# Kernel tuning notes

Measured on AMD Instinct MI355X. Metric: run time of the kernel, lower is better.

Reference implementation:

```python
import jax, jax.numpy as jnp
import numpy as np

D_MODEL = 1024
N_HEADS = 16
WINDOW = 64
GLOBAL_RATIO = 0.1
HEAD_DIM = D_MODEL // N_HEADS
NEG_INF = -1e9  # matches torch float32 branch of _get_neg_inf
B, L = 1, 2048


def setup_inputs() -> dict:
    key = jax.random.key(0)
    ks = jax.random.split(key, 6)
    x = jax.random.normal(ks[0], (B, L, D_MODEL), jnp.float32)
    s = 1.0 / np.sqrt(D_MODEL)  # nn.Linear default init bound

    def lin(k):
        k1, k2 = jax.random.split(k)
        W = jax.random.uniform(k1, (D_MODEL, D_MODEL), jnp.float32, -s, s)
        b = jax.random.uniform(k2, (D_MODEL,), jnp.float32, -s, s)
        return W, b

    Wq, bq = lin(ks[1])
    Wk, bk = lin(ks[2])
    Wv, bv = lin(ks[3])
    Wo, bo = lin(ks[4])
    n_global = max(1, int(L * GLOBAL_RATIO))  # 204
    global_indices = jnp.sort(jax.random.randint(ks[5], (n_global,), 0, L))
    return dict(x=x, Wq=Wq, bq=bq, Wk=Wk, bk=bk, Wv=Wv, bv=bv, Wo=Wo, bo=bo,
                global_indices=global_indices)


def reference(x, Wq, bq, Wk, bk, Wv, bv, Wo, bo, global_indices):
    Bb, Ll, Dm = x.shape
    H, Dh = N_HEADS, HEAD_DIM
    scale = 1.0 / jnp.sqrt(jnp.float32(Dh))
    # projections (torch Linear: y = x @ W.T + b)
    Q = (x @ Wq.T + bq).reshape(Bb, Ll, H, Dh)
    K = (x @ Wk.T + bk).reshape(Bb, Ll, H, Dh)
    V = (x @ Wv.T + bv).reshape(Bb, Ll, H, Dh)

    # --- local sliding-window attention (vectorized version of the per-i loop) ---
    half = WINDOW // 2
    W = WINDOW + 1  # positions i-half .. i+half inclusive
    pos = jnp.arange(Ll)[:, None] + jnp.arange(-half, half + 1)[None, :]  # [L,W]
    valid = (pos >= 0) & (pos < Ll)          # edge truncation == masking to -inf
    posc = jnp.clip(pos, 0, Ll - 1)
    Kw = K[:, posc]                           # [B,L,W,H,Dh]
    Vw = V[:, posc]
    s_loc = jnp.einsum('blhd,blwhd->bhlw', Q, Kw) * scale
    s_loc = jnp.where(valid[None, None], s_loc, NEG_INF)
    a_loc = jax.nn.softmax(s_loc, axis=-1)
    local = jnp.einsum('bhlw,blwhd->blhd', a_loc, Vw)

    # --- global random-token attention ---
    Kg = K[:, global_indices]                 # [B,G,H,Dh]
    Vg = V[:, global_indices]
    s_g = jnp.einsum('blhd,bghd->bhlg', Q, Kg) * scale
    a_g = jax.nn.softmax(s_g, axis=-1)
    glob = jnp.einsum('bhlg,bghd->blhd', a_g, Vg)

    out = 0.7 * local + 0.3 * glob
    return out.reshape(Bb, Ll, Dm) @ Wo.T + bo
```

## Files before the change

kernel.cpp:

```cpp
#include <hip/hip_runtime.h>
#include <hip/hip_bf16.h>
#include <stdint.h>

#define L_SEQ 2048
#define D_MODEL 1024
#define NH 16
#define DH 64
#define NEG_INF -1e9f

typedef short bf16x4 __attribute__((ext_vector_type(4)));
typedef short bf16x8 __attribute__((ext_vector_type(8)));
typedef float f32x4 __attribute__((ext_vector_type(4)));
typedef unsigned short ushort_t;
typedef const __attribute__((address_space(1))) void* gas_t;
typedef __attribute__((address_space(3))) void* las_t;

#define MFMA16(a, b, c) __builtin_amdgcn_mfma_f32_16x16x32_bf16((a), (b), (c), 0, 0, 0)

__device__ __forceinline__ ushort_t f2b(float f) {
  union { float f; unsigned u; } v; v.f = f;
  unsigned r = v.u + 0x7fffu + ((v.u >> 16) & 1u);
  return (ushort_t)(r >> 16);
}
__device__ __forceinline__ float b2f(ushort_t u) {
  union { unsigned u; float f; } v; v.u = ((unsigned)u) << 16; return v.f;
}

__global__ __launch_bounds__(256) void cvt_kernel(
    const float* __restrict__ x, const float* __restrict__ wq,
    const float* __restrict__ wk, const float* __restrict__ wv,
    const float* __restrict__ wo, ushort_t* __restrict__ out) {
  long e = ((long)blockIdx.x * 256 + threadIdx.x) * 4;
  const float* src; long off;
  if (e < 2097152L)      { src = x;  off = e; }
  else if (e < 3145728L) { src = wq; off = e - 2097152L; }
  else if (e < 4194304L) { src = wk; off = e - 3145728L; }
  else if (e < 5242880L) { src = wv; off = e - 4194304L; }
  else                   { src = wo; off = e - 5242880L; }
  float4 v = *(const float4*)(src + off);
  ushort4 o;
  o.x = f2b(v.x); o.y = f2b(v.y); o.z = f2b(v.z); o.w = f2b(v.w);
  *(ushort4*)(out + e) = o;
}

__global__ __launch_bounds__(512, 4) void gemm_qkv(
    const ushort_t* __restrict__ A, const ushort_t* __restrict__ Wbase,
    const float* __restrict__ b0, const float* __restrict__ b1,
    const float* __restrict__ b2, ushort_t* __restrict__ outbase) {
  const int z = blockIdx.z;
  const ushort_t* W = Wbase + (long)z * (D_MODEL * D_MODEL);
  const float* bias = (z == 0) ? b0 : ((z == 1) ? b1 : b2);
  const float scale = (z == 0) ? 0.125f : 1.0f;

  __shared__ ushort_t As[4 * 128 * 32];
  __shared__ ushort_t Bs[4 * 128 * 32];
  const int tid = threadIdx.x;
  const int lane = tid & 63;
  const int wid = tid >> 6;
  const int wm = wid >> 2, wn = wid & 3;
  const int m0 = blockIdx.x * 128, n0 = blockIdx.y * 128;
  const int K = D_MODEL;
  const int l15 = lane & 15;
  const int lgc = lane >> 4;
  const int xs = (l15 >> 1) & 3;

  const int soff = tid * 16;
  const int srow = soff >> 6;
  const int schunk = (soff >> 4) & 3;
  const int swzcol = ((schunk ^ ((srow >> 1) & 3)) << 3);

  const ushort_t* Aptr = A + (long)(m0 + srow) * K + swzcol;
  const ushort_t* Wptr = W + (long)(n0 + srow) * K + swzcol;

  auto stage = [&](int buf, int step) {
    __builtin_amdgcn_global_load_lds(
        (gas_t)(const void*)(Aptr + step * 32),
        (las_t)(void*)((char*)As + buf * 8192 + soff), 16, 0, 0);
    __builtin_amdgcn_global_load_lds(
        (gas_t)(const void*)(Wptr + step * 32),
        (las_t)(void*)((char*)Bs + buf * 8192 + soff), 16, 0, 0);
  };

  f32x4 acc[4][2] = {};

  auto compute = [&](int buf) {
    const ushort_t* Ab = As + buf * (128 * 32);
    const ushort_t* Bb = Bs + buf * (128 * 32);
    bf16x8 af[4], bf[2];
#pragma unroll
    for (int t = 0; t < 4; ++t)
      af[t] = *(const bf16x8*)(Ab + (wm * 64 + t * 16 + l15) * 32 +
                               ((lgc ^ xs) << 3));
#pragma unroll
    for (int t = 0; t < 2; ++t)
      bf[t] = *(const bf16x8*)(Bb + (wn * 32 + t * 16 + l15) * 32 +
                               ((lgc ^ xs) << 3));
#pragma unroll
    for (int mt = 0; mt < 4; ++mt)
#pragma unroll
      for (int nt = 0; nt < 2; ++nt)
        acc[mt][nt] = MFMA16(af[mt], bf[nt], acc[mt][nt]);
  };

  const int NSTEP = K / 32;
  stage(0, 0);
  stage(1, 1);
  for (int s = 0; s < NSTEP - 2; ++s) {
    stage((s + 2) & 3, s + 2);
    asm volatile("s_waitcnt vmcnt(4)" ::: "memory");
    __builtin_amdgcn_s_barrier();
    __builtin_amdgcn_sched_barrier(0);
    compute(s & 3);
  }
  asm volatile("s_waitcnt vmcnt(2)" ::: "memory");
  __builtin_amdgcn_s_barrier();
  __builtin_amdgcn_sched_barrier(0);
  compute((NSTEP - 2) & 3);
  asm volatile("s_waitcnt vmcnt(0)" ::: "memory");
  __builtin_amdgcn_s_barrier();
  __builtin_amdgcn_sched_barrier(0);
  compute((NSTEP - 1) & 3);

  const int lg4 = (lane >> 4) * 4;
  ushort_t* o = outbase + (long)z * ((long)NH * L_SEQ * DH);
#pragma unroll
  for (int mt = 0; mt < 4; ++mt)
#pragma unroll
    for (int nt = 0; nt < 2; ++nt)
#pragma unroll
      for (int r = 0; r < 4; ++r) {
        int row = m0 + wm * 64 + mt * 16 + lg4 + r;
        int col = n0 + wn * 32 + nt * 16 + l15;
        float v = (acc[mt][nt][r] + bias[col]) * scale;
        o[((long)(col >> 6) * L_SEQ + row) * DH + (col & 63)] = f2b(v);
      }
}

__global__ __launch_bounds__(256, 3) void gemm_out(
    const ushort_t* __restrict__ A, const ushort_t* __restrict__ W,
    const float* __restrict__ bias, float* __restrict__ o) {
  __shared__ ushort_t As[4 * 128 * 32];
  __shared__ ushort_t Bs[4 * 64 * 32];
  const int tid = threadIdx.x;
  const int lane = tid & 63;
  const int wid = tid >> 6;
  const int wm = wid >> 1, wn = wid & 1;
  const int m0 = blockIdx.x * 128, n0 = blockIdx.y * 64;
  const int K = D_MODEL;
  const int l15 = lane & 15;
  const int lgc = lane >> 4;
  const int xs = (l15 >> 1) & 3;

  const int soff = tid * 16;
  const int srow = soff >> 6;
  const int schunk = (soff >> 4) & 3;
  const int swzcol = ((schunk ^ ((srow >> 1) & 3)) << 3);

  const ushort_t* Aptr0 = A + (long)(m0 + srow) * K + swzcol;
  const ushort_t* Aptr1 = A + (long)(m0 + 64 + srow) * K + swzcol;
  const ushort_t* Wptr  = W + (long)(n0 + srow) * K + swzcol;

  auto stage = [&](int buf, int step) {
    __builtin_amdgcn_global_load_lds(
        (gas_t)(const void*)(Aptr0 + step * 32),
        (las_t)(void*)((char*)As + buf * 8192 + soff), 16, 0, 0);
    __builtin_amdgcn_global_load_lds(
        (gas_t)(const void*)(Aptr1 + step * 32),
        (las_t)(void*)((char*)As + buf * 8192 + 4096 + soff), 16, 0, 0);
    __builtin_amdgcn_global_load_lds(
        (gas_t)(const void*)(Wptr + step * 32),
        (las_t)(void*)((char*)Bs + buf * 4096 + soff), 16, 0, 0);
  };

  f32x4 acc[4][2] = {};

  auto compute = [&](int buf) {
    const ushort_t* Ab = As + buf * (128 * 32);
    const ushort_t* Bb = Bs + buf * (64 * 32);
    bf16x8 af[4], bf[2];
#pragma unroll
    for (int t = 0; t < 4; ++t)
      af[t] = *(const bf16x8*)(Ab + (wm * 64 + t * 16 + l15) * 32 +
                               ((lgc ^ xs) << 3));
#pragma unroll
    for (int t = 0; t < 2; ++t)
      bf[t] = *(const bf16x8*)(Bb + (wn * 32 + t * 16 + l15) * 32 +
                               ((lgc ^ xs) << 3));
#pragma unroll
    for (int mt = 0; mt < 4; ++mt)
#pragma unroll
      for (int nt = 0; nt < 2; ++nt)
        acc[mt][nt] = MFMA16(af[mt], bf[nt], acc[mt][nt]);
  };

  const int NSTEP = K / 32;
  stage(0, 0);
  stage(1, 1);
  for (int s = 0; s < NSTEP - 2; ++s) {
    stage((s + 2) & 3, s + 2);
    asm volatile("s_waitcnt vmcnt(6)" ::: "memory");
    __builtin_amdgcn_s_barrier();
    __builtin_amdgcn_sched_barrier(0);
    compute(s & 3);
  }
  asm volatile("s_waitcnt vmcnt(3)" ::: "memory");
  __builtin_amdgcn_s_barrier();
  __builtin_amdgcn_sched_barrier(0);
  compute((NSTEP - 2) & 3);
  asm volatile("s_waitcnt vmcnt(0)" ::: "memory");
  __builtin_amdgcn_s_barrier();
  __builtin_amdgcn_sched_barrier(0);
  compute((NSTEP - 1) & 3);

  const int lg4 = (lane >> 4) * 4;
#pragma unroll
  for (int mt = 0; mt < 4; ++mt)
#pragma unroll
    for (int nt = 0; nt < 2; ++nt)
#pragma unroll
      for (int r = 0; r < 4; ++r) {
        int row = m0 + wm * 64 + mt * 16 + lg4 + r;
        int col = n0 + wn * 32 + nt * 16 + l15;
        o[(long)row * D_MODEL + col] = acc[mt][nt][r] + bias[col];
      }
}

__global__ __launch_bounds__(256) void attn_local(
    const ushort_t* __restrict__ QKV, ushort_t* __restrict__ attnL) {
  __shared__ ushort_t kb[128 * 72];
  __shared__ ushort_t vt[64 * 132];

  const int tid = threadIdx.x;
  const int lane = tid & 63;
  const int w = tid >> 6;
  const int h = blockIdx.y;
  const int q0 = blockIdx.x * 64;

  const long hoff = (long)h * L_SEQ * DH;
  const ushort_t* Qh = QKV + hoff;
  const ushort_t* Kh = QKV + (long)NH * L_SEQ * DH + hoff;
  const ushort_t* Vh = QKV + 2L * NH * L_SEQ * DH + hoff;

  const int rr = tid >> 3;
  const int c8 = (tid & 7) * 8;
  const int l15 = lane & 15, lg = lane >> 4;
  const int ql = q0 + w * 16 + l15;

  int4 vst[4];
#pragma unroll
  for (int it = 0; it < 4; ++it) {
    int r = rr + it * 32;
    int sr = q0 - 32 + r;
    sr = sr < 0 ? 0 : (sr > L_SEQ - 1 ? L_SEQ - 1 : sr);
    vst[it] = *(const int4*)(Vh + (long)sr * DH + c8);
  }
  bf16x8 qf0 = *(const bf16x8*)(Qh + (long)ql * DH + lg * 8);
  bf16x8 qf1 = *(const bf16x8*)(Qh + (long)ql * DH + 32 + lg * 8);

#pragma unroll
  for (int it = 0; it < 4; ++it) {
    int r = rr + it * 32;
    int sr = q0 - 32 + r;
    sr = sr < 0 ? 0 : (sr > L_SEQ - 1 ? L_SEQ - 1 : sr);
    int4 v = *(const int4*)(Kh + (long)sr * DH + c8);
    *(int4*)(kb + r * 72 + c8) = v;
  }
  __syncthreads();

  f32x4 sl[5];
#pragma unroll
  for (int kt = 0; kt < 5; ++kt) {
    f32x4 c = {};
    const ushort_t* kr = kb + (w * 16 + kt * 16 + l15) * 72;
    bf16x8 k0 = *(const bf16x8*)(kr + lg * 8);
    bf16x8 k1 = *(const bf16x8*)(kr + 32 + lg * 8);
    c = MFMA16(k0, qf0, c);
    c = MFMA16(k1, qf1, c);
    sl[kt] = c;
  }

  float mx = NEG_INF;
#pragma unroll
  for (int kt = 0; kt < 5; ++kt)
#pragma unroll
    for (int r4 = 0; r4 < 4; ++r4) {
      int key = q0 - 32 + w * 16 + kt * 16 + lg * 4 + r4;
      int d = key - ql;
      bool valid = (key >= 0) && (key < L_SEQ) && (d <= 32) && (d >= -32);
      float v = valid ? sl[kt][r4] : NEG_INF;
      sl[kt][r4] = v;
      mx = fmaxf(mx, v);
    }
  mx = fmaxf(mx, __shfl_xor(mx, 16, 64));
  mx = fmaxf(mx, __shfl_xor(mx, 32, 64));
  float den = 0.f;
#pragma unroll
  for (int kt = 0; kt < 5; ++kt)
#pragma unroll
    for (int r4 = 0; r4 < 4; ++r4) {
      float e = __expf(sl[kt][r4] - mx);
      sl[kt][r4] = e;
      den += e;
    }
  den += __shfl_xor(den, 16, 64);
  den += __shfl_xor(den, 32, 64);
  const float psl = 0.7f / den;

  bf16x8 pl[3];
#pragma unroll
  for (int s = 0; s < 2; ++s)
#pragma unroll
    for (int j = 0; j < 4; ++j) {
      pl[s][j]     = (short)f2b(sl[2 * s][j] * psl);
      pl[s][j + 4] = (short)f2b(sl[2 * s + 1][j] * psl);
    }
#pragma unroll
  for (int j = 0; j < 4; ++j) {
    pl[2][j]     = (short)f2b(sl[4][j] * psl);
    pl[2][j + 4] = 0;
  }

#pragma unroll
  for (int it = 0; it < 4; ++it) {
    int r = rr + it * 32;
    ushort_t tmp[8]; *(int4*)tmp = vst[it];
#pragma unroll
    for (int j = 0; j < 8; ++j) vt[(c8 + j) * 132 + r] = tmp[j];
  }
  __syncthreads();

#pragma unroll
  for (int dt = 0; dt < 4; ++dt) {
    f32x4 c = {};
    const ushort_t* vrow = vt + (dt * 16 + l15) * 132 + w * 16 + lg * 4;
#pragma unroll
    for (int s = 0; s < 3; ++s) {
      bf16x4 lo = *(const bf16x4*)(vrow + s * 32);
      bf16x4 hi = *(const bf16x4*)(vrow + s * 32 + (s < 2 ? 16 : 0));
      bf16x8 vf = __builtin_shufflevector(lo, hi, 0, 1, 2, 3, 4, 5, 6, 7);
      c = MFMA16(pl[s], vf, c);
    }
#pragma unroll
    for (int r4 = 0; r4 < 4; ++r4) {
      int row = q0 + w * 16 + lg * 4 + r4;
      attnL[(long)row * D_MODEL + h * DH + dt * 16 + l15] = f2b(c[r4]);
    }
  }
}

#define VTW 228
__global__ __launch_bounds__(512) void attn_glob(
    const ushort_t* __restrict__ QKV, const int* __restrict__ gidx, int NG,
    const ushort_t* __restrict__ attnL, ushort_t* __restrict__ attn_out) {
  __shared__ ushort_t kg[208 * 72];
  __shared__ ushort_t vtg[64 * VTW];

  const int tid = threadIdx.x;
  const int lane = tid & 63;
  const int w = tid >> 6;
  const int h = blockIdx.y;
  const int q0 = blockIdx.x * 128;

  const long hoff = (long)h * L_SEQ * DH;
  const ushort_t* Qh = QKV + hoff;
  const ushort_t* Kh = QKV + (long)NH * L_SEQ * DH + hoff;
  const ushort_t* Vh = QKV + 2L * NH * L_SEQ * DH + hoff;

  const int l15 = lane & 15, lg = lane >> 4;
  const int ql = q0 + w * 16 + l15;

  int4 vst[4];
#pragma unroll
  for (int it = 0; it < 4; ++it) {
    int c = tid + it * 512;
    int cl = c < 1664 ? c : 1663;
    int r = cl >> 3, cc = (cl & 7) * 8;
    int idx = r < NG ? r : NG - 1;
    vst[it] = *(const int4*)(Vh + (long)gidx[idx] * DH + cc);
  }
  bf16x8 qf0 = *(const bf16x8*)(Qh + (long)ql * DH + lg * 8);
  bf16x8 qf1 = *(const bf16x8*)(Qh + (long)ql * DH + 32 + lg * 8);
  ushort_t aL[4][4];
#pragma unroll
  for (int dt = 0; dt < 4; ++dt)
#pragma unroll
    for (int r4 = 0; r4 < 4; ++r4) {
      int row = q0 + w * 16 + lg * 4 + r4;
      aL[dt][r4] = attnL[(long)row * D_MODEL + h * DH + dt * 16 + l15];
    }

#pragma unroll
  for (int it = 0; it < 4; ++it) {
    int c = tid + it * 512;
    if (c < 1664) {
      int r = c >> 3, cc = (c & 7) * 8;
      int idx = r < NG ? r : NG - 1;
      int4 v = *(const int4*)(Kh + (long)gidx[idx] * DH + cc);
      *(int4*)(kg + r * 72 + cc) = v;
    }
  }
  __syncthreads();

  f32x4 sg[13];
#pragma unroll
  for (int kt = 0; kt < 13; ++kt) {
    f32x4 c = {};
    bf16x8 k0 = *(const bf16x8*)(kg + (kt * 16 + l15) * 72 + lg * 8);
    bf16x8 k1 = *(const bf16x8*)(kg + (kt * 16 + l15) * 72 + 32 + lg * 8);
    c = MFMA16(k0, qf0, c);
    c = MFMA16(k1, qf1, c);
    sg[kt] = c;
  }

  float mg = NEG_INF;
#pragma unroll
  for (int t = 0; t < 13; ++t)
#pragma unroll
    for (int r4 = 0; r4 < 4; ++r4) {
      int i = t * 16 + lg * 4 + r4;
      float v = (i < NG) ? sg[t][r4] : NEG_INF;
      sg[t][r4] = v;
      mg = fmaxf(mg, v);
    }
  mg = fmaxf(mg, __shfl_xor(mg, 16, 64));
  mg = fmaxf(mg, __shfl_xor(mg, 32, 64));
  float deng = 0.f;
#pragma unroll
  for (int t = 0; t < 13; ++t)
#pragma unroll
    for (int r4 = 0; r4 < 4; ++r4) {
      float e = __expf(sg[t][r4] - mg);
      sg[t][r4] = e;
      deng += e;
    }
  deng += __shfl_xor(deng, 16, 64);
  deng += __shfl_xor(deng, 32, 64);
  const float psg = 0.3f / deng;

  bf16x8 pg[7];
#pragma unroll
  for (int s = 0; s < 6; ++s)
#pragma unroll
    for (int j = 0; j < 4; ++j) {
      pg[s][j]     = (short)f2b(sg[2 * s][j] * psg);
      pg[s][j + 4] = (short)f2b(sg[2 * s + 1][j] * psg);
    }
#pragma unroll
  for (int j = 0; j < 4; ++j) {
    pg[6][j]     = (short)f2b(sg[12][j] * psg);
    pg[6][j + 4] = 0;
  }

#pragma unroll
  for (int it = 0; it < 4; ++it) {
    int c = tid + it * 512;
    if (c < 1664) {
      int r = c >> 3, cc = (c & 7) * 8;
      ushort_t tmp[8]; *(int4*)tmp = vst[it];
#pragma unroll
      for (int j = 0; j < 8; ++j) vtg[(cc + j) * VTW + r] = tmp[j];
    }
  }
  for (int i = tid; i < 64 * 20; i += 512)
    vtg[(i / 20) * VTW + 208 + (i % 20)] = 0;
  __syncthreads();

#pragma unroll
  for (int dt = 0; dt < 4; ++dt) {
    f32x4 c = {};
    const ushort_t* vrow = vtg + (dt * 16 + l15) * VTW + lg * 4;
#pragma unroll
    for (int s = 0; s < 7; ++s) {
      bf16x4 lo = *(const bf16x4*)(vrow + s * 32);
      bf16x4 hi = *(const bf16x4*)(vrow + s * 32 + 16);
      bf16x8 vf = __builtin_shufflevector(lo, hi, 0, 1, 2, 3, 4, 5, 6, 7);
      c = MFMA16(pg[s], vf, c);
    }
#pragma unroll
    for (int r4 = 0; r4 < 4; ++r4) {
      int row = q0 + w * 16 + lg * 4 + r4;
      long off = (long)row * D_MODEL + h * DH + dt * 16 + l15;
      attn_out[off] = f2b(b2f(aL[dt][r4]) + c[r4]);
    }
  }
}

extern "C" void kernel_launch(void* const* d_in, const int* in_sizes, int n_in,
                              void* d_out, int out_size, void* d_ws, size_t ws_size,
                              hipStream_t stream) {
  const float* x  = (const float*)d_in[0];
  const float* Wq = (const float*)d_in[1];
  const float* bq = (const float*)d_in[2];
  const float* Wk = (const float*)d_in[3];
  const float* bk = (const float*)d_in[4];
  const float* Wv = (const float*)d_in[5];
  const float* bv = (const float*)d_in[6];
  const float* Wo = (const float*)d_in[7];
  const float* bo = (const float*)d_in[8];
  const int* gidx = (const int*)d_in[9];
  const int NG = in_sizes[9];

  ushort_t* ws = (ushort_t*)d_ws;
  ushort_t* xb    = ws;
  ushort_t* wb    = ws + 2097152L;
  ushort_t* qkv   = ws + 6291456L;
  ushort_t* attn  = ws + 12582912L;
  ushort_t* attnL = ws + 14680064L;

  cvt_kernel<<<6144, 256, 0, stream>>>(x, Wq, Wk, Wv, Wo, ws);
  gemm_qkv<<<dim3(16, 8, 3), 512, 0, stream>>>(xb, wb, bq, bk, bv, qkv);
  attn_local<<<dim3(32, 16), 256, 0, stream>>>(qkv, attnL);
  attn_glob<<<dim3(16, 16), 512, 0, stream>>>(qkv, gidx, NG, attnL, attn);
  gemm_out<<<dim3(16, 16), 256, 0, stream>>>(attn, wb + 3145728L, bo,
                                             (float*)d_out);
}
```

Baseline: 63.08 us.

## Fuse local and global attention into one kernel sharing Q and accumulator

Merges the separate local-window and global-token attention kernels into a single kernel of 128 queries per block. Q is loaded once, both score sets are computed, and both P·V products accumulate into the same MFMA accumulator. This drops the intermediate attnL bf16 round trip through global memory and one kernel launch. In exchange it uses more registers (sl and sg live at once) and reuses a 57.6KB shared buffer for K and then V, which needs an extra barrier.

Result: faster. 60.31 us (-4.4%).

```diff
diff --git a/kernel.cpp b/kernel.cpp
--- a/kernel.cpp
+++ b/kernel.cpp
@@ -21,9 +21,6 @@
   union { float f; unsigned u; } v; v.f = f;
   unsigned r = v.u + 0x7fffu + ((v.u >> 16) & 1u);
   return (ushort_t)(r >> 16);
-}
-__device__ __forceinline__ float b2f(ushort_t u) {
-  union { unsigned u; float f; } v; v.u = ((unsigned)u) << 16; return v.f;
 }
 
 __global__ __launch_bounds__(256) void cvt_kernel(
@@ -225,45 +222,70 @@
       }
 }
 
-__global__ __launch_bounds__(256) void attn_local(
-    const ushort_t* __restrict__ QKV, ushort_t* __restrict__ attnL) {
-  __shared__ ushort_t kb[128 * 72];
-  __shared__ ushort_t vt[64 * 132];
+#define VTW 228
+__global__ __launch_bounds__(512) void attn_fused(
+    const ushort_t* __restrict__ QKV, const int* __restrict__ gidx, int NG,
+    ushort_t* __restrict__ attn_out) {
+  __shared__ ushort_t smem[28800];
 
   const int tid = threadIdx.x;
   const int lane = tid & 63;
   const int w = tid >> 6;
   const int h = blockIdx.y;
-  const int q0 = blockIdx.x * 64;
+  const int q0 = blockIdx.x * 128;
 
   const long hoff = (long)h * L_SEQ * DH;
   const ushort_t* Qh = QKV + hoff;
   const ushort_t* Kh = QKV + (long)NH * L_SEQ * DH + hoff;
   const ushort_t* Vh = QKV + 2L * NH * L_SEQ * DH + hoff;
 
-  const int rr = tid >> 3;
-  const int c8 = (tid & 7) * 8;
   const int l15 = lane & 15, lg = lane >> 4;
   const int ql = q0 + w * 16 + l15;
 
-  int4 vst[4];
-#pragma unroll
-  for (int it = 0; it < 4; ++it) {
-    int r = rr + it * 32;
+  ushort_t* kl = smem;
+  ushort_t* kg = smem + 192 * 72;
+  ushort_t* vtl = smem;
+  ushort_t* vtg = smem + 64 * 196;
+
+  int4 vstL[3];
+#pragma unroll
+  for (int it = 0; it < 3; ++it) {
+    int c = tid + it * 512;
+    int r = c >> 3, cc = (c & 7) * 8;
     int sr = q0 - 32 + r;
     sr = sr < 0 ? 0 : (sr > L_SEQ - 1 ? L_SEQ - 1 : sr);
-    vst[it] = *(const int4*)(Vh + (long)sr * DH + c8);
+    vstL[it] = *(const int4*)(Vh + (long)sr * DH + cc);
+  }
+  int4 vstG[4];
+#pragma unroll
+  for (int it = 0; it < 4; ++it) {
+    int c = tid + it * 512;
+    int cl = c < 1664 ? c : 1663;
+    int r = cl >> 3, cc = (cl & 7) * 8;
+    int idx = r < NG ? r : NG - 1;
+    vstG[it] = *(const int4*)(Vh + (long)gidx[idx] * DH + cc);
   }
   bf16x8 qf0 = *(const bf16x8*)(Qh + (long)ql * DH + lg * 8);
   bf16x8 qf1 = *(const bf16x8*)(Qh + (long)ql * DH + 32 + lg * 8);
 
 #pragma unroll
-  for (int it = 0; it < 4; ++it) {
-    int r = rr + it * 32;
+  for (int it = 0; it < 3; ++it) {
+    int c = tid + it * 512;
+    int r = c >> 3, cc = (c & 7) * 8;
     int sr = q0 - 32 + r;
     sr = sr < 0 ? 0 : (sr > L_SEQ - 1 ? L_SEQ - 1 : sr);
-    int4 v = *(const int4*)(Kh + (long)sr * DH + c8);
-    *(int4*)(kb + r * 72 + c8) = v;
+    int4 v = *(const int4*)(Kh + (long)sr * DH + cc);
+    *(int4*)(kl + r * 72 + cc) = v;
+  }
+#pragma unroll
+  for (int it = 0; it < 4; ++it) {
+    int c = tid + it * 512;
+    if (c < 1664) {
+      int r = c >> 3, cc = (c & 7) * 8;
+      int idx = r < NG ? r : NG - 1;
+      int4 v = *(const int4*)(Kh + (long)gidx[idx] * DH + cc);
+      *(int4*)(kg + r * 72 + cc) = v;
+    }
   }
   __syncthreads();
 
@@ -271,13 +293,45 @@
 #pragma unroll
   for (int kt = 0; kt < 5; ++kt) {
     f32x4 c = {};
-    const ushort_t* kr = kb + (w * 16 + kt * 16 + l15) * 72;
+    const ushort_t* kr = kl + (w * 16 + kt * 16 + l15) * 72;
     bf16x8 k0 = *(const bf16x8*)(kr + lg * 8);
     bf16x8 k1 = *(const bf16x8*)(kr + 32 + lg * 8);
     c = MFMA16(k0, qf0, c);
     c = MFMA16(k1, qf1, c);
     sl[kt] = c;
   }
+  f32x4 sg[13];
+#pragma unroll
+  for (int kt = 0; kt < 13; ++kt) {
+    f32x4 c = {};
+    bf16x8 k0 = *(const bf16x8*)(kg + (kt * 16 + l15) * 72 + lg * 8);
+    bf16x8 k1 = *(const bf16x8*)(kg + (kt * 16 + l15) * 72 + 32 + lg * 8);
+    c = MFMA16(k0, qf0, c);
+    c = MFMA16(k1, qf1, c);
+    sg[kt] = c;
+  }
+  __syncthreads();
+
+#pragma unroll
+  for (int it = 0; it < 3; ++it) {
+    int c = tid + it * 512;
+    int r = c >> 3, cc = (c & 7) * 8;
+    ushort_t tmp[8]; *(int4*)tmp = vstL[it];
+#pragma unroll
+    for (int j = 0; j < 8; ++j) vtl[(cc + j) * 196 + r] = tmp[j];
+  }
+#pragma unroll
+  for (int it = 0; it < 4; ++it) {
+    int c = tid + it * 512;
+    if (c < 1664) {
+      int r = c >> 3, cc = (c & 7) * 8;
+      ushort_t tmp[8]; *(int4*)tmp = vstG[it];
+#pragma unroll
+      for (int j = 0; j < 8; ++j) vtg[(cc + j) * VTW + r] = tmp[j];
+    }
+  }
+  for (int i = tid; i < 64 * 20; i += 512)
+    vtg[(i / 20) * VTW + 208 + (i % 20)] = 0;
 
   float mx = NEG_INF;
 #pragma unroll
@@ -306,112 +360,6 @@
   den += __shfl_xor(den, 32, 64);
   const float psl = 0.7f / den;
 
-  bf16x8 pl[3];
-#pragma unroll
-  for (int s = 0; s < 2; ++s)
-#pragma unroll
-    for (int j = 0; j < 4; ++j) {
-      pl[s][j]     = (short)f2b(sl[2 * s][j] * psl);
-      pl[s][j + 4] = (short)f2b(sl[2 * s + 1][j] * psl);
-    }
-#pragma unroll
-  for (int j = 0; j < 4; ++j) {
-    pl[2][j]     = (short)f2b(sl[4][j] * psl);
-    pl[2][j + 4] = 0;
-  }
-
-#pragma unroll
-  for (int it = 0; it < 4; ++it) {
-    int r = rr + it * 32;
-    ushort_t tmp[8]; *(int4*)tmp = vst[it];
-#pragma unroll
-    for (int j = 0; j < 8; ++j) vt[(c8 + j) * 132 + r] = tmp[j];
-  }
-  __syncthreads();
-
-#pragma unroll
-  for (int dt = 0; dt < 4; ++dt) {
-    f32x4 c = {};
-    const ushort_t* vrow = vt + (dt * 16 + l15) * 132 + w * 16 + lg * 4;
-#pragma unroll
-    for (int s = 0; s < 3; ++s) {
-      bf16x4 lo = *(const bf16x4*)(vrow + s * 32);
-      bf16x4 hi = *(const bf16x4*)(vrow + s * 32 + (s < 2 ? 16 : 0));
-      bf16x8 vf = __builtin_shufflevector(lo, hi, 0, 1, 2, 3, 4, 5, 6, 7);
-      c = MFMA16(pl[s], vf, c);
-    }
-#pragma unroll
-    for (int r4 = 0; r4 < 4; ++r4) {
-      int row = q0 + w * 16 + lg * 4 + r4;
-      attnL[(long)row * D_MODEL + h * DH + dt * 16 + l15] = f2b(c[r4]);
-    }
-  }
-}
-
-#define VTW 228
-__global__ __launch_bounds__(512) void attn_glob(
-    const ushort_t* __restrict__ QKV, const int* __restrict__ gidx, int NG,
-    const ushort_t* __restrict__ attnL, ushort_t* __restrict__ attn_out) {
-  __shared__ ushort_t kg[208 * 72];
-  __shared__ ushort_t vtg[64 * VTW];
-
-  const int tid = threadIdx.x;
-  const int lane = tid & 63;
-  const int w = tid >> 6;
-  const int h = blockIdx.y;
-  const int q0 = blockIdx.x * 128;
-
-  const long hoff = (long)h * L_SEQ * DH;
-  const ushort_t* Qh = QKV + hoff;
-  const ushort_t* Kh = QKV + (long)NH * L_SEQ * DH + hoff;
-  const ushort_t* Vh = QKV + 2L * NH * L_SEQ * DH + hoff;
-
-  const int l15 = lane & 15, lg = lane >> 4;
-  const int ql = q0 + w * 16 + l15;
-
-  int4 vst[4];
-#pragma unroll
-  for (int it = 0; it < 4; ++it) {
-    int c = tid + it * 512;
-    int cl = c < 1664 ? c : 1663;
-    int r = cl >> 3, cc = (cl & 7) * 8;
-    int idx = r < NG ? r : NG - 1;
-    vst[it] = *(const int4*)(Vh + (long)gidx[idx] * DH + cc);
-  }
-  bf16x8 qf0 = *(const bf16x8*)(Qh + (long)ql * DH + lg * 8);
-  bf16x8 qf1 = *(const bf16x8*)(Qh + (long)ql * DH + 32 + lg * 8);
-  ushort_t aL[4][4];
-#pragma unroll
-  for (int dt = 0; dt < 4; ++dt)
-#pragma unroll
-    for (int r4 = 0; r4 < 4; ++r4) {
-      int row = q0 + w * 16 + lg * 4 + r4;
-      aL[dt][r4] = attnL[(long)row * D_MODEL + h * DH + dt * 16 + l15];
-    }
-
-#pragma unroll
-  for (int it = 0; it < 4; ++it) {
-    int c = tid + it * 512;
-    if (c < 1664) {
-      int r = c >> 3, cc = (c & 7) * 8;
-      int idx = r < NG ? r : NG - 1;
-      int4 v = *(const int4*)(Kh + (long)gidx[idx] * DH + cc);
-      *(int4*)(kg + r * 72 + cc) = v;
-    }
-  }
-  __syncthreads();
-
-  f32x4 sg[13];
-#pragma unroll
-  for (int kt = 0; kt < 13; ++kt) {
-    f32x4 c = {};
-    bf16x8 k0 = *(const bf16x8*)(kg + (kt * 16 + l15) * 72 + lg * 8);
-    bf16x8 k1 = *(const bf16x8*)(kg + (kt * 16 + l15) * 72 + 32 + lg * 8);
-    c = MFMA16(k0, qf0, c);
-    c = MFMA16(k1, qf1, c);
-    sg[kt] = c;
-  }
-
   float mg = NEG_INF;
 #pragma unroll
   for (int t = 0; t < 13; ++t)
@@ -437,6 +385,19 @@
   deng += __shfl_xor(deng, 32, 64);
   const float psg = 0.3f / deng;
 
+  bf16x8 pl[3];
+#pragma unroll
+  for (int s = 0; s < 2; ++s)
+#pragma unroll
+    for (int j = 0; j < 4; ++j) {
+      pl[s][j]     = (short)f2b(sl[2 * s][j] * psl);
+      pl[s][j + 4] = (short)f2b(sl[2 * s + 1][j] * psl);
+    }
+#pragma unroll
+  for (int j = 0; j < 4; ++j) {
+    pl[2][j]     = (short)f2b(sl[4][j] * psl);
+    pl[2][j + 4] = 0;
+  }
   bf16x8 pg[7];
 #pragma unroll
   for (int s = 0; s < 6; ++s)
@@ -450,37 +411,31 @@
     pg[6][j]     = (short)f2b(sg[12][j] * psg);
     pg[6][j + 4] = 0;
   }
-
-#pragma unroll
-  for (int it = 0; it < 4; ++it) {
-    int c = tid + it * 512;
-    if (c < 1664) {
-      int r = c >> 3, cc = (c & 7) * 8;
-      ushort_t tmp[8]; *(int4*)tmp = vst[it];
-#pragma unroll
-      for (int j = 0; j < 8; ++j) vtg[(cc + j) * VTW + r] = tmp[j];
-    }
-  }
-  for (int i = tid; i < 64 * 20; i += 512)
-    vtg[(i / 20) * VTW + 208 + (i % 20)] = 0;
   __syncthreads();
 
 #pragma unroll
   for (int dt = 0; dt < 4; ++dt) {
     f32x4 c = {};
-    const ushort_t* vrow = vtg + (dt * 16 + l15) * VTW + lg * 4;
+    const ushort_t* vrowL = vtl + (dt * 16 + l15) * 196 + w * 16 + lg * 4;
+#pragma unroll
+    for (int s = 0; s < 3; ++s) {
+      bf16x4 lo = *(const bf16x4*)(vrowL + s * 32);
+      bf16x4 hi = *(const bf16x4*)(vrowL + s * 32 + (s < 2 ? 16 : 0));
+      bf16x8 vf = __builtin_shufflevector(lo, hi, 0, 1, 2, 3, 4, 5, 6, 7);
+      c = MFMA16(pl[s], vf, c);
+    }
+    const ushort_t* vrowG = vtg + (dt * 16 + l15) * VTW + lg * 4;
 #pragma unroll
     for (int s = 0; s < 7; ++s) {
-      bf16x4 lo = *(const bf16x4*)(vrow + s * 32);
-      bf16x4 hi = *(const bf16x4*)(vrow + s * 32 + 16);
+      bf16x4 lo = *(const bf16x4*)(vrowG + s * 32);
+      bf16x4 hi = *(const bf16x4*)(vrowG + s * 32 + 16);
       bf16x8 vf = __builtin_shufflevector(lo, hi, 0, 1, 2, 3, 4, 5, 6, 7);
       c = MFMA16(pg[s], vf, c);
     }
 #pragma unroll
     for (int r4 = 0; r4 < 4; ++r4) {
       int row = q0 + w * 16 + lg * 4 + r4;
-      long off = (long)row * D_MODEL + h * DH + dt * 16 + l15;
-      attn_out[off] = f2b(b2f(aL[dt][r4]) + c[r4]);
+      attn_out[(long)row * D_MODEL + h * DH + dt * 16 + l15] = f2b(c[r4]);
     }
   }
 }
@@ -505,12 +460,10 @@
   ushort_t* wb    = ws + 2097152L;
   ushort_t* qkv   = ws + 6291456L;
   ushort_t* attn  = ws + 12582912L;
-  ushort_t* attnL = ws + 14680064L;
 
   cvt_kernel<<<6144, 256, 0, stream>>>(x, Wq, Wk, Wv, Wo, ws);
   gemm_qkv<<<dim3(16, 8, 3), 512, 0, stream>>>(xb, wb, bq, bk, bv, qkv);
-  attn_local<<<dim3(32, 16), 256, 0, stream>>>(qkv, attnL);
-  attn_glob<<<dim3(16, 16), 512, 0, stream>>>(qkv, gidx, NG, attnL, attn);
+  attn_fused<<<dim3(16, 16), 512, 0, stream>>>(qkv, gidx, NG, attn);
   gemm_out<<<dim3(16, 16), 256, 0, stream>>>(attn, wb + 3145728L, bo,
                                              (float*)d_out);
 }
```
